# Kernel tuning notes

Hardware: AMD Instinct MI355X
Metric: run time of the kernel (lower is better)

## Reference

```python
import jax, jax.numpy as jnp
import numpy as np

S, B, V, E, H = 1024, 64, 32000, 512, 512
PAD = 0


def _ln3(x, g, b, eps=1e-5):
    # LayerNorm applied per-gate: x is (..., 3H); normalize over each H chunk.
    h = x.shape[-1] // 3
    xr = x.reshape(x.shape[:-1] + (3, h))
    mu = xr.mean(-1, keepdims=True)
    var = xr.var(-1, keepdims=True)
    xn = (xr - mu) * jax.lax.rsqrt(var + eps)
    out = xn * g.reshape(3, h) + b.reshape(3, h)
    return out.reshape(x.shape)


def _gru_dir(x, Wih, Whh, bih, bhh, gih, beih, ghh, behh, reverse):
    # x: (S, B, E). Precompute all input projections at once (big GEMM),
    # then scan the recurrence.
    xp = _ln3(jnp.einsum('sbe,ge->sbg', x, Wih), gih, beih) + bih  # (S,B,3H)

    def step(h, xt):
        hp = _ln3(h @ Whh.T, ghh, behh) + bhh  # (B,3H)
        xr, xz, xn = jnp.split(xt, 3, axis=-1)
        hr, hz, hn = jnp.split(hp, 3, axis=-1)
        r = jax.nn.sigmoid(xr + hr)
        z = jax.nn.sigmoid(xz + hz)
        n = jnp.tanh(xn + r * hn)
        hnew = (1.0 - z) * n + z * h
        return hnew, hnew

    h0 = jnp.zeros((x.shape[1], Whh.shape[1]), x.dtype)
    hT, ys = jax.lax.scan(step, h0, xp, reverse=reverse)
    return ys, hT  # ys in original time order for both directions


def setup_inputs() -> dict:
    key = jax.random.key(0)
    ks = jax.random.split(key, 8)
    sE = 1.0 / np.sqrt(E)
    sH = 1.0 / np.sqrt(H)
    z3 = jnp.zeros((3 * H,), jnp.float32)
    o3 = jnp.ones((3 * H,), jnp.float32)
    return {
        'src': jax.random.randint(ks[0], (S, B), 0, V, dtype=jnp.int32),
        'emb': jax.random.normal(ks[1], (V, E), jnp.float32),
        'W_ih_f': jax.random.normal(ks[2], (3 * H, E), jnp.float32) * sE,
        'W_hh_f': jax.random.normal(ks[3], (3 * H, H), jnp.float32) * sH,
        'b_ih_f': z3, 'b_hh_f': z3,
        'g_ih_f': o3, 'be_ih_f': z3, 'g_hh_f': o3, 'be_hh_f': z3,
        'W_ih_b': jax.random.normal(ks[4], (3 * H, E), jnp.float32) * sE,
        'W_hh_b': jax.random.normal(ks[5], (3 * H, H), jnp.float32) * sH,
        'b_ih_b': z3, 'b_hh_b': z3,
        'g_ih_b': o3, 'be_ih_b': z3, 'g_hh_b': o3, 'be_hh_b': z3,
        'W_out': jax.random.normal(ks[6], (H, 2 * H), jnp.float32) * (1.0 / np.sqrt(2 * H)),
        'b_out': jnp.zeros((H,), jnp.float32),
    }


def reference(src, emb, W_ih_f, W_hh_f, b_ih_f, b_hh_f, g_ih_f, be_ih_f,
              g_hh_f, be_hh_f, W_ih_b, W_hh_b, b_ih_b, b_hh_b, g_ih_b,
              be_ih_b, g_hh_b, be_hh_b, W_out, b_out):
    # Embedding with padding_idx=0 (padding row contributes zeros).
    x = emb[src] * (src != PAD)[..., None].astype(emb.dtype)  # (S,B,E)
    # embedding_dropout = dropout = 0.0 -> identity (eval semantics)
    yf, hf = _gru_dir(x, W_ih_f, W_hh_f, b_ih_f, b_hh_f,
                      g_ih_f, be_ih_f, g_hh_f, be_hh_f, reverse=False)
    yb, hb = _gru_dir(x, W_ih_b, W_hh_b, b_ih_b, b_hh_b,
                      g_ih_b, be_ih_b, g_hh_b, be_hh_b, reverse=True)
    gru_out = jnp.concatenate([yf, yb], axis=-1)  # (S,B,2H)
    outputs = jnp.tanh(gru_out @ W_out.T + b_out)  # (S,B,H)
    hidden = jnp.stack([hf, hb], axis=0)  # (2,B,H)
    return outputs, hidden
```

## Files before the change

### kernel.cpp

```cpp
#include <hip/hip_runtime.h>
#include <hip/hip_bf16.h>
#include <hip/hip_fp16.h>

#define S_ 1024
#define B_ 64
#define E_ 512
#define H_ 512
#define G3_ 1536

typedef __hip_bfloat16 bf16;
typedef __half f16;
typedef unsigned long long ULL;

template<typename T> struct alignas(4*sizeof(T)) V4 { T v[4]; };

__device__ __forceinline__ float toF(float x){ return x; }
__device__ __forceinline__ float toF(bf16 x){ return __bfloat162float(x); }
__device__ __forceinline__ float toF(f16 x){ return __half2float(x); }
__device__ __forceinline__ void storeF(float* p, float v){ *p = v; }
__device__ __forceinline__ void storeF(bf16* p, float v){ *p = __float2bfloat16(v); }
__device__ __forceinline__ void storeF(f16* p, float v){ *p = __float2half(v); }

__device__ __forceinline__ ULL cohLoad8(const ULL* p){
  return __hip_atomic_load(p, __ATOMIC_RELAXED, __HIP_MEMORY_SCOPE_AGENT);
}
__device__ __forceinline__ void cohStore4(float* p, float v){
  __hip_atomic_store(p, v, __ATOMIC_RELAXED, __HIP_MEMORY_SCOPE_AGENT);
}
__device__ __forceinline__ unsigned flagLoad(const unsigned* p){
  return __hip_atomic_load(p, __ATOMIC_RELAXED, __HIP_MEMORY_SCOPE_AGENT);
}
__device__ __forceinline__ void flagStore(unsigned* p, unsigned v){
  __hip_atomic_store(p, v, __ATOMIC_RELAXED, __HIP_MEMORY_SCOPE_AGENT);
}

__global__ __launch_bounds__(256)
void signal_kernel(float* __restrict__ out, long n, float v)
{
  long i = (long)blockIdx.x * 256 + threadIdx.x;
  const long stride = (long)gridDim.x * 256;
  for (; i < n; i += stride) out[i] = v;
}

template<typename XT, typename HT, int AMODE, int EPI>
__global__ __launch_bounds__(256, 2)
void gemm_tile(const int* __restrict__ src, const float* __restrict__ emb,
               const HT* __restrict__ Af, int rsF, const XT* __restrict__ Ab, int rsB,
               const float* __restrict__ W,
               XT* __restrict__ Cx, float* __restrict__ Cf, const float* __restrict__ bias,
               int N, int K)
{
  __shared__ float As[16][132];
  __shared__ float Bs[16][132];
  __shared__ int s_tok[128];
  const int m0 = blockIdx.x * 128;
  const int n0 = blockIdx.y * 128;
  const int tid = threadIdx.x;
  const int tx = tid & 15, ty = tid >> 4;

  if constexpr (AMODE == 0) {
    if (tid < 128) s_tok[tid] = src[m0 + tid];
  }
  __syncthreads();

  float acc[8][8];
  #pragma unroll
  for (int i = 0; i < 8; ++i)
    #pragma unroll
    for (int j = 0; j < 8; ++j) acc[i][j] = 0.f;

  for (int k0 = 0; k0 < K; k0 += 16) {
    #pragma unroll
    for (int i = 0; i < 2; ++i) {
      const int f = tid * 2 + i;
      const int r = f >> 2, kq = f & 3;
      const int kk = k0 + kq * 4;
      float a0, a1, a2, a3;
      if constexpr (AMODE == 0) {
        const int tok = s_tok[r];
        if (tok != 0) {
          float4 v = *(const float4*)(emb + (size_t)tok * E_ + kk);
          a0 = v.x; a1 = v.y; a2 = v.z; a3 = v.w;
        } else { a0 = a1 = a2 = a3 = 0.f; }
      } else {
        if (kk < H_) {
          V4<HT> v = *(const V4<HT>*)(Af + (size_t)(m0 + r) * rsF + kk);
          a0 = toF(v.v[0]); a1 = toF(v.v[1]); a2 = toF(v.v[2]); a3 = toF(v.v[3]);
        } else {
          V4<XT> v = *(const V4<XT>*)(Ab + (size_t)(m0 + r) * rsB + (kk - H_));
          a0 = toF(v.v[0]); a1 = toF(v.v[1]); a2 = toF(v.v[2]); a3 = toF(v.v[3]);
        }
      }
      As[kq*4+0][r] = a0; As[kq*4+1][r] = a1; As[kq*4+2][r] = a2; As[kq*4+3][r] = a3;
      float4 b = *(const float4*)(W + (size_t)(n0 + r) * K + kk);
      Bs[kq*4+0][r] = b.x; Bs[kq*4+1][r] = b.y; Bs[kq*4+2][r] = b.z; Bs[kq*4+3][r] = b.w;
    }
    __syncthreads();
    #pragma unroll
    for (int k = 0; k < 16; ++k) {
      float4 ra0 = *(const float4*)&As[k][ty*8];
      float4 ra1 = *(const float4*)&As[k][ty*8+4];
      float4 rb0 = *(const float4*)&Bs[k][tx*8];
      float4 rb1 = *(const float4*)&Bs[k][tx*8+4];
      float fa[8] = {ra0.x,ra0.y,ra0.z,ra0.w,ra1.x,ra1.y,ra1.z,ra1.w};
      float fb[8] = {rb0.x,rb0.y,rb0.z,rb0.w,rb1.x,rb1.y,rb1.z,rb1.w};
      #pragma unroll
      for (int i = 0; i < 8; ++i)
        #pragma unroll
        for (int j = 0; j < 8; ++j) acc[i][j] += fa[i] * fb[j];
    }
    __syncthreads();
  }

  if constexpr (EPI == 0) {
    #pragma unroll
    for (int i = 0; i < 8; ++i) {
      XT* crow = Cx + (size_t)(m0 + ty*8 + i) * N + n0 + tx*8;
      V4<XT> o0, o1;
      #pragma unroll
      for (int c = 0; c < 4; ++c) { storeF(&o0.v[c], acc[i][c]); storeF(&o1.v[c], acc[i][4+c]); }
      ((V4<XT>*)crow)[0] = o0; ((V4<XT>*)crow)[1] = o1;
    }
  } else {
    float bj[8];
    #pragma unroll
    for (int j = 0; j < 8; ++j) bj[j] = bias[n0 + tx*8 + j];
    #pragma unroll
    for (int i = 0; i < 8; ++i) {
      float* crow = Cf + (size_t)(m0 + ty*8 + i) * N + n0 + tx*8;
      float4 o0, o1;
      o0.x = tanhf(acc[i][0]+bj[0]); o0.y = tanhf(acc[i][1]+bj[1]);
      o0.z = tanhf(acc[i][2]+bj[2]); o0.w = tanhf(acc[i][3]+bj[3]);
      o1.x = tanhf(acc[i][4]+bj[4]); o1.y = tanhf(acc[i][5]+bj[5]);
      o1.z = tanhf(acc[i][6]+bj[6]); o1.w = tanhf(acc[i][7]+bj[7]);
      ((float4*)crow)[0] = o0; ((float4*)crow)[1] = o1;
    }
  }
}

template<typename XT>
__global__ __launch_bounds__(256)
void ln3_kernel(XT* __restrict__ xp, const float* __restrict__ g,
                const float* __restrict__ be, const float* __restrict__ b)
{
  const size_t base = (size_t)blockIdx.x * G3_;
  const int t = threadIdx.x;
  float v[6];
  #pragma unroll
  for (int gg = 0; gg < 3; ++gg) {
    v[gg*2+0] = toF(xp[base + gg*512 + t]);
    v[gg*2+1] = toF(xp[base + gg*512 + 256 + t]);
  }
  float s0 = v[0]+v[1], q0 = v[0]*v[0]+v[1]*v[1];
  float s1 = v[2]+v[3], q1 = v[2]*v[2]+v[3]*v[3];
  float s2 = v[4]+v[5], q2 = v[4]*v[4]+v[5]*v[5];
  #pragma unroll
  for (int m = 1; m < 64; m <<= 1) {
    s0 += __shfl_xor(s0, m); q0 += __shfl_xor(q0, m);
    s1 += __shfl_xor(s1, m); q1 += __shfl_xor(q1, m);
    s2 += __shfl_xor(s2, m); q2 += __shfl_xor(q2, m);
  }
  __shared__ float red[4][6];
  __shared__ float stat[6];
  const int wid = t >> 6, lane = t & 63;
  if (lane == 0) { red[wid][0]=s0; red[wid][1]=q0; red[wid][2]=s1; red[wid][3]=q1; red[wid][4]=s2; red[wid][5]=q2; }
  __syncthreads();
  if (t < 6) stat[t] = red[0][t] + red[1][t] + red[2][t] + red[3][t];
  __syncthreads();
  #pragma unroll
  for (int gg = 0; gg < 3; ++gg) {
    const float mu  = stat[gg*2]   * (1.f/512.f);
    const float var = stat[gg*2+1] * (1.f/512.f) - mu*mu;
    const float sc  = rsqrtf(var + 1e-5f);
    #pragma unroll
    for (int u = 0; u < 2; ++u) {
      const int c = gg*512 + u*256 + t;
      storeF(&xp[base + c], (v[gg*2+u] - mu) * sc * g[c] + be[c] + b[c]);
    }
  }
}

template<typename XT, typename HT>
__global__ __launch_bounds__(256, 2)
void scan_kernel(const XT* __restrict__ xp_f, const XT* __restrict__ xp_b,
                 const float* __restrict__ Whh_f, const float* __restrict__ Whh_b,
                 const float* __restrict__ gf, const float* __restrict__ bef, const float* __restrict__ bfv,
                 const float* __restrict__ gbv, const float* __restrict__ beb, const float* __restrict__ bbv,
                 float* __restrict__ hbuf, float* __restrict__ part,
                 unsigned* __restrict__ flags,
                 HT* __restrict__ houtF, int rsF, XT* __restrict__ houtB, int rsB,
                 float* __restrict__ outhid, int dirbase)
{
  __shared__ float hT[8][512];
  __shared__ float red[4][16][26];
  __shared__ float statL[48];
  __shared__ int sdead;

  const int bid  = blockIdx.x;
  const int gidx = dirbase*8 + (bid >> 5);
  const int dir  = gidx >> 3;
  const int bg   = gidx & 7;
  const int js   = bid & 31;
  const int tid  = threadIdx.x;
  const int jloc = tid & 15;
  const int pb   = tid >> 4;
  const int wid  = tid >> 6;
  const int ksw  = (tid >> 4) & 3;
  const int j    = js*16 + jloc;

  const XT* xp   = dir ? xp_b : xp_f;
  const float* W = dir ? Whh_b : Whh_f;
  const float* gv  = dir ? gbv : gf;
  const float* bev = dir ? beb : bef;
  const float* bv  = dir ? bbv : bfv;
  float* h = hbuf + dir * (B_ * H_);
  float* pgrp = part + (size_t)gidx * (48*32);
  unsigned* hfl = flags + (size_t)gidx * 2048;
  unsigned* sfl = hfl + 1024;

  if (tid == 0) sdead = 0;

  float w[3][32];
  {
    #pragma unroll
    for (int r = 0; r < 3; ++r) {
      const float* wr = W + (size_t)(r*H_ + j) * H_ + pb * 32;
      #pragma unroll
      for (int c = 0; c < 8; ++c) {
        const int p = (c + ksw*2) & 7;
        float4 f = *(const float4*)(wr + p*4);
        w[r][c*4+0] = f.x; w[r][c*4+1] = f.y; w[r][c*4+2] = f.z; w[r][c*4+3] = f.w;
      }
    }
  }
  const float gr0 = gv[j],            gr1 = gv[H_+j],               gr2 = gv[2*H_+j];
  const float gb0 = bev[j] + bv[j],   gb1 = bev[H_+j] + bv[H_+j],   gb2 = bev[2*H_+j] + bv[2*H_+j];
  __syncthreads();

  for (int t = 0; t < S_; ++t) {
    const int tf = dir ? (S_ - 1 - t) : t;
    float xr = 0.f, xz = 0.f, xn = 0.f;
    if (pb < 8) {
      const size_t xbase = ((size_t)tf * B_ + bg*8 + pb) * G3_;
      xr = toF(xp[xbase + j]);
      xz = toF(xp[xbase + H_ + j]);
      xn = toF(xp[xbase + 2*H_ + j]);
    }

    if (tid < 32 && !sdead) {
      const unsigned tgt = (unsigned)t;
      int guard = 0;
      while (flagLoad(&hfl[tid*32]) < tgt) {
        __builtin_amdgcn_s_sleep(1);
        if (++guard > (1 << 22)) { sdead = 1; break; }
      }
    }
    __syncthreads();

    {
      const int row = tid >> 5;
      const int seg = tid & 31;
      const ULL* hr = (const ULL*)(h + (size_t)(bg*8 + row) * H_);
      ULL v[8];
      #pragma unroll
      for (int i = 0; i < 8; ++i) v[i] = cohLoad8(hr + seg + i*32);
      ULL* dst = (ULL*)&hT[row][0];
      #pragma unroll
      for (int i = 0; i < 8; ++i) dst[seg + i*32] = v[i];
    }
    __syncthreads();

    for (int b = 0; b < 8; ++b) {
      float a0 = 0.f, a1 = 0.f, a2 = 0.f;
      #pragma unroll
      for (int c = 0; c < 8; ++c) {
        const int p = (c + ksw*2) & 7;
        const float4 hv = *(const float4*)&hT[b][pb*32 + p*4];
        a0 += hv.x*w[0][c*4+0] + hv.y*w[0][c*4+1] + hv.z*w[0][c*4+2] + hv.w*w[0][c*4+3];
        a1 += hv.x*w[1][c*4+0] + hv.y*w[1][c*4+1] + hv.z*w[1][c*4+2] + hv.w*w[1][c*4+3];
        a2 += hv.x*w[2][c*4+0] + hv.y*w[2][c*4+1] + hv.z*w[2][c*4+2] + hv.w*w[2][c*4+3];
      }
      a0 += __shfl_xor(a0, 16); a0 += __shfl_xor(a0, 32);
      a1 += __shfl_xor(a1, 16); a1 += __shfl_xor(a1, 32);
      a2 += __shfl_xor(a2, 16); a2 += __shfl_xor(a2, 32);
      if (ksw == 0) {
        red[wid][jloc][b*3+0] = a0; red[wid][jloc][b*3+1] = a1; red[wid][jloc][b*3+2] = a2;
      }
    }
    __syncthreads();

    float vr = 0.f, vz = 0.f, vn = 0.f;
    if (pb < 8) {
      vr = red[0][jloc][pb*3+0]+red[1][jloc][pb*3+0]+red[2][jloc][pb*3+0]+red[3][jloc][pb*3+0];
      vz = red[0][jloc][pb*3+1]+red[1][jloc][pb*3+1]+red[2][jloc][pb*3+1]+red[3][jloc][pb*3+1];
      vn = red[0][jloc][pb*3+2]+red[1][jloc][pb*3+2]+red[2][jloc][pb*3+2]+red[3][jloc][pb*3+2];

      float sr = vr, qr = vr*vr, sz = vz, qz = vz*vz, sn = vn, qn = vn*vn;
      #pragma unroll
      for (int m = 1; m < 16; m <<= 1) {
        sr += __shfl_xor(sr, m); qr += __shfl_xor(qr, m);
        sz += __shfl_xor(sz, m); qz += __shfl_xor(qz, m);
        sn += __shfl_xor(sn, m); qn += __shfl_xor(qn, m);
      }
      if (jloc == 0) {
        cohStore4(&pgrp[(pb*6+0)*32 + js], sr);
        cohStore4(&pgrp[(pb*6+1)*32 + js], qr);
        cohStore4(&pgrp[(pb*6+2)*32 + js], sz);
        cohStore4(&pgrp[(pb*6+3)*32 + js], qz);
        cohStore4(&pgrp[(pb*6+4)*32 + js], sn);
        cohStore4(&pgrp[(pb*6+5)*32 + js], qn);
      }
    }
    asm volatile("s_waitcnt vmcnt(0)" ::: "memory");
    __syncthreads();

    if (tid == 0) flagStore(&sfl[js*32], (unsigned)(t + 1));
    if (tid < 32 && !sdead) {
      const unsigned tgt = (unsigned)(t + 1);
      int guard = 0;
      while (flagLoad(&sfl[tid*32]) < tgt) {
        __builtin_amdgcn_s_sleep(1);
        if (++guard > (1 << 22)) { sdead = 1; break; }
      }
    }
    __syncthreads();

    if (tid < 48) {
      const ULL* prow = (const ULL*)(pgrp + tid * 32);
      float s = 0.f;
      #pragma unroll
      for (int u = 0; u < 16; ++u) {
        ULL v = cohLoad8(prow + u);
        union { ULL u64; float f[2]; } cv; cv.u64 = v;
        s += cv.f[0] + cv.f[1];
      }
      statL[tid] = s;
    }
    __syncthreads();

    if (pb < 8) {
      const int ab = bg*8 + pb;
      const float mur   = statL[pb*6+0]*(1.f/512.f);
      const float var_r = statL[pb*6+1]*(1.f/512.f) - mur*mur;
      const float muz   = statL[pb*6+2]*(1.f/512.f);
      const float var_z = statL[pb*6+3]*(1.f/512.f) - muz*muz;
      const float mun   = statL[pb*6+4]*(1.f/512.f);
      const float var_n = statL[pb*6+5]*(1.f/512.f) - mun*mun;
      const float hr_ = (vr - mur) * rsqrtf(var_r + 1e-5f) * gr0 + gb0;
      const float hz_ = (vz - muz) * rsqrtf(var_z + 1e-5f) * gr1 + gb1;
      const float hn_ = (vn - mun) * rsqrtf(var_n + 1e-5f) * gr2 + gb2;
      const float rg = 1.f / (1.f + __expf(-(xr + hr_)));
      const float zg = 1.f / (1.f + __expf(-(xz + hz_)));
      const float ng = tanhf(xn + rg * hn_);
      const float hprev = hT[pb][j];
      const float hnew = (1.f - zg) * ng + zg * hprev;
      cohStore4(&h[(size_t)ab * H_ + j], hnew);
      if (dir == 0) storeF(&houtF[((size_t)tf * B_ + ab) * rsF + j], hnew);
      else          storeF(&houtB[((size_t)tf * B_ + ab) * rsB + j], hnew);
      if (t == S_ - 1) outhid[((size_t)dir * B_ + ab) * H_ + j] = hnew;
    }
    asm volatile("s_waitcnt vmcnt(0)" ::: "memory");
    __syncthreads();
    if (tid == 0) flagStore(&hfl[js*32], (unsigned)(t + 1));
  }
}

static const size_t kCtrlBytes = 524288;
static const size_t kXpElems = (size_t)S_ * B_ * G3_;
static const size_t kHElems  = (size_t)S_ * B_ * H_;

struct Args {
  const int* src; const float* emb;
  const float *Wih_f, *Whh_f, *bih_f, *bhh_f, *gih_f, *beih_f, *ghh_f, *behh_f;
  const float *Wih_b, *Whh_b, *bih_b, *bhh_b, *gih_b, *beih_b, *ghh_b, *behh_b;
  const float *Wout, *bout;
  float* out; void* ws; hipStream_t stream;
};

template<typename XT>
static void run_parallel(const Args& a)
{
  float* hbuf = (float*)a.ws;
  float* part = hbuf + 65536;
  unsigned* flags = (unsigned*)(part + 24576);
  XT* xpf = (XT*)((char*)a.ws + kCtrlBytes);
  XT* xpb = xpf + kXpElems;
  float* outhid = a.out + kHElems;

  hipMemsetAsync(a.ws, 0, kCtrlBytes, a.stream);

  gemm_tile<XT,XT,0,0><<<dim3(512,12), dim3(256), 0, a.stream>>>(
      a.src, a.emb, (const XT*)nullptr, 0, (const XT*)nullptr, 0,
      a.Wih_f, xpf, nullptr, nullptr, G3_, E_);
  gemm_tile<XT,XT,0,0><<<dim3(512,12), dim3(256), 0, a.stream>>>(
      a.src, a.emb, (const XT*)nullptr, 0, (const XT*)nullptr, 0,
      a.Wih_b, xpb, nullptr, nullptr, G3_, E_);
  ln3_kernel<XT><<<dim3(S_*B_), dim3(256), 0, a.stream>>>(xpf, a.gih_f, a.beih_f, a.bih_f);
  ln3_kernel<XT><<<dim3(S_*B_), dim3(256), 0, a.stream>>>(xpb, a.gih_b, a.beih_b, a.bih_b);

  scan_kernel<XT,XT><<<dim3(512), dim3(256), 0, a.stream>>>(
      xpf, xpb, a.Whh_f, a.Whh_b, a.ghh_f, a.behh_f, a.bhh_f,
      a.ghh_b, a.behh_b, a.bhh_b, hbuf, part, flags,
      xpf, G3_, xpb, G3_, outhid, 0);

  gemm_tile<XT,XT,1,1><<<dim3(512,4), dim3(256), 0, a.stream>>>(
      nullptr, nullptr, xpf, G3_, xpb, G3_,
      a.Wout, (XT*)nullptr, a.out, a.bout, H_, 2*H_);
}

template<typename XT, typename HT>
static void run_sequential(const Args& a)
{
  float* hbuf = (float*)a.ws;
  float* part = hbuf + 65536;
  unsigned* flags = (unsigned*)(part + 24576);
  XT* xp = (XT*)((char*)a.ws + kCtrlBytes);
  HT* hf = (HT*)(xp + kXpElems);
  float* outhid = a.out + kHElems;

  hipMemsetAsync(a.ws, 0, kCtrlBytes, a.stream);

  gemm_tile<XT,XT,0,0><<<dim3(512,12), dim3(256), 0, a.stream>>>(
      a.src, a.emb, (const XT*)nullptr, 0, (const XT*)nullptr, 0,
      a.Wih_f, xp, nullptr, nullptr, G3_, E_);
  ln3_kernel<XT><<<dim3(S_*B_), dim3(256), 0, a.stream>>>(xp, a.gih_f, a.beih_f, a.bih_f);
  scan_kernel<XT,HT><<<dim3(256), dim3(256), 0, a.stream>>>(
      xp, xp, a.Whh_f, a.Whh_b, a.ghh_f, a.behh_f, a.bhh_f,
      a.ghh_b, a.behh_b, a.bhh_b, hbuf, part, flags,
      hf, H_, xp, G3_, outhid, 0);

  gemm_tile<XT,XT,0,0><<<dim3(512,12), dim3(256), 0, a.stream>>>(
      a.src, a.emb, (const XT*)nullptr, 0, (const XT*)nullptr, 0,
      a.Wih_b, xp, nullptr, nullptr, G3_, E_);
  ln3_kernel<XT><<<dim3(S_*B_), dim3(256), 0, a.stream>>>(xp, a.gih_b, a.beih_b, a.bih_b);
  scan_kernel<XT,HT><<<dim3(256), dim3(256), 0, a.stream>>>(
      xp, xp, a.Whh_f, a.Whh_b, a.ghh_f, a.behh_f, a.bhh_f,
      a.ghh_b, a.behh_b, a.bhh_b, hbuf, part, flags,
      hf, H_, xp, G3_, outhid, 1);

  gemm_tile<XT,HT,1,1><<<dim3(512,4), dim3(256), 0, a.stream>>>(
      nullptr, nullptr, hf, H_, xp, G3_,
      a.Wout, (XT*)nullptr, a.out, a.bout, H_, 2*H_);
}

extern "C" void kernel_launch(void* const* d_in, const int* in_sizes, int n_in,
                              void* d_out, int out_size, void* d_ws, size_t ws_size,
                              hipStream_t stream)
{
  Args a;
  a.src    = (const int*)  d_in[0];
  a.emb    = (const float*)d_in[1];
  a.Wih_f  = (const float*)d_in[2];
  a.Whh_f  = (const float*)d_in[3];
  a.bih_f  = (const float*)d_in[4];
  a.bhh_f  = (const float*)d_in[5];
  a.gih_f  = (const float*)d_in[6];
  a.beih_f = (const float*)d_in[7];
  a.ghh_f  = (const float*)d_in[8];
  a.behh_f = (const float*)d_in[9];
  a.Wih_b  = (const float*)d_in[10];
  a.Whh_b  = (const float*)d_in[11];
  a.bih_b  = (const float*)d_in[12];
  a.bhh_b  = (const float*)d_in[13];
  a.gih_b  = (const float*)d_in[14];
  a.beih_b = (const float*)d_in[15];
  a.ghh_b  = (const float*)d_in[16];
  a.behh_b = (const float*)d_in[17];
  a.Wout   = (const float*)d_in[18];
  a.bout   = (const float*)d_in[19];
  a.out = (float*)d_out;
  a.ws = d_ws;
  a.stream = stream;

  int dev = 0, cus = 0;
  hipGetDevice(&dev);
  hipDeviceGetAttribute(&cus, hipDeviceAttributeMultiprocessorCount, dev);

  const size_t needP = kCtrlBytes + 2*kXpElems*2;
  const size_t needS = kCtrlBytes + kXpElems*2 + kHElems*2;

  const bool sane = (n_in == 20) && (in_sizes[0] == S_*B_) && (in_sizes[1] == 32000*E_)
                 && (in_sizes[3] == G3_*H_) && (in_sizes[18] == H_*2*H_);

  float sigv = 0.f;
  bool ran = false;
  if (!sane) {
    sigv = 20000.f + (float)n_in;
  } else if (cus < 256) {
    sigv = 100000.f + (float)cus;
  } else if (ws_size >= needP) { run_parallel<f16>(a);        ran = true; }
  else if (ws_size >= needS) { run_sequential<f16,f16>(a);    ran = true; }
  else {
    unsigned wsMB = (unsigned)(ws_size >> 20);
    if (wsMB > 998) wsMB = 998;
    sigv = 1000.f + (float)wsMB;
  }

  if (!ran) {
    signal_kernel<<<dim3(1024), dim3(256), 0, stream>>>(a.out, (long)out_size, sigv);
  } else {
    hipError_t e = hipGetLastError();
    if (e != hipSuccess) {
      signal_kernel<<<dim3(1024), dim3(256), 0, stream>>>(a.out, (long)out_size,
                                                          10000.f + (float)(int)e);
    }
  }
}
```

Before: 13.34 ms.

## Replace FP32 SIMT GEMMs with FP16 MFMA GEMMs over pre-converted weights

Adds a conversion kernel that casts the embedding table, input-projection weights and output weights to fp16 in workspace on every call. The GEMM is rewritten to feed half8 fragments straight from global memory into 16x16x32 f16 MFMA instructions, with no shared-memory staging. This targets the FP32 FMA cost of the input-projection and output GEMMs. In exchange it adds per-call conversion traffic (the embedding table is large), needs a bigger workspace, loses precision by using fp16 operands, and its uncoalesced scalar epilogue stores may be slow.

```diff
diff --git a/kernel.cpp b/kernel.cpp
--- a/kernel.cpp
+++ b/kernel.cpp
@@ -7,10 +7,14 @@
 #define E_ 512
 #define H_ 512
 #define G3_ 1536
+#define V_ 32000
 
 typedef __hip_bfloat16 bf16;
 typedef __half f16;
 typedef unsigned long long ULL;
+
+typedef _Float16 half8 __attribute__((ext_vector_type(8)));
+typedef float f32x4v __attribute__((ext_vector_type(4)));
 
 template<typename T> struct alignas(4*sizeof(T)) V4 { T v[4]; };
 
@@ -42,98 +46,120 @@
   for (; i < n; i += stride) out[i] = v;
 }
 
-template<typename XT, typename HT, int AMODE, int EPI>
-__global__ __launch_bounds__(256, 2)
-void gemm_tile(const int* __restrict__ src, const float* __restrict__ emb,
-               const HT* __restrict__ Af, int rsF, const XT* __restrict__ Ab, int rsB,
-               const float* __restrict__ W,
-               XT* __restrict__ Cx, float* __restrict__ Cf, const float* __restrict__ bias,
-               int N, int K)
-{
-  __shared__ float As[16][132];
-  __shared__ float Bs[16][132];
+__global__ __launch_bounds__(256)
+void convF2H(const float* __restrict__ in, f16* __restrict__ out, long n)
+{
+  long i = ((long)blockIdx.x * 256 + threadIdx.x) * 8;
+  const long stride = (long)gridDim.x * 256 * 8;
+  for (; i < n; i += stride) {
+    float4 a = *(const float4*)(in + i);
+    float4 b = *(const float4*)(in + i + 4);
+    half8 o;
+    o[0] = (_Float16)a.x; o[1] = (_Float16)a.y; o[2] = (_Float16)a.z; o[3] = (_Float16)a.w;
+    o[4] = (_Float16)b.x; o[5] = (_Float16)b.y; o[6] = (_Float16)b.z; o[7] = (_Float16)b.w;
+    *(half8*)((_Float16*)out + i) = o;
+  }
+}
+
+template<int GMODE, int EPI>
+__global__ __launch_bounds__(256)
+void gemm16(const int* __restrict__ src, const f16* __restrict__ embh,
+            const f16* __restrict__ Af, int rsF,
+            const f16* __restrict__ Ab, int rsB,
+            const f16* __restrict__ Wh,
+            f16* __restrict__ Cx, float* __restrict__ Cf,
+            const float* __restrict__ bias, int N, int K)
+{
   __shared__ int s_tok[128];
+  const int tid = threadIdx.x;
   const int m0 = blockIdx.x * 128;
   const int n0 = blockIdx.y * 128;
-  const int tid = threadIdx.x;
-  const int tx = tid & 15, ty = tid >> 4;
-
-  if constexpr (AMODE == 0) {
+  const int wid = tid >> 6, lane = tid & 63;
+  const int wr = wid >> 1, wc = wid & 1;
+  const int lr = lane & 15, lg = lane >> 4;
+
+  if constexpr (GMODE == 0) {
     if (tid < 128) s_tok[tid] = src[m0 + tid];
   }
   __syncthreads();
 
-  float acc[8][8];
+  f32x4v acc[4][4];
   #pragma unroll
-  for (int i = 0; i < 8; ++i)
-    #pragma unroll
-    for (int j = 0; j < 8; ++j) acc[i][j] = 0.f;
-
-  for (int k0 = 0; k0 < K; k0 += 16) {
-    #pragma unroll
-    for (int i = 0; i < 2; ++i) {
-      const int f = tid * 2 + i;
-      const int r = f >> 2, kq = f & 3;
-      const int kk = k0 + kq * 4;
-      float a0, a1, a2, a3;
-      if constexpr (AMODE == 0) {
-        const int tok = s_tok[r];
-        if (tok != 0) {
-          float4 v = *(const float4*)(emb + (size_t)tok * E_ + kk);
-          a0 = v.x; a1 = v.y; a2 = v.z; a3 = v.w;
-        } else { a0 = a1 = a2 = a3 = 0.f; }
+  for (int i = 0; i < 4; ++i)
+    #pragma unroll
+    for (int j = 0; j < 4; ++j) {
+      acc[i][j][0] = 0.f; acc[i][j][1] = 0.f; acc[i][j][2] = 0.f; acc[i][j][3] = 0.f;
+    }
+
+  int atok[4]; size_t abase[4];
+  #pragma unroll
+  for (int i = 0; i < 4; ++i) {
+    const int lm = wr*64 + i*16 + lr;
+    if constexpr (GMODE == 0) {
+      const int tok = s_tok[lm];
+      atok[i] = tok;
+      abase[i] = (size_t)tok * K;
+    } else {
+      atok[i] = m0 + lm;
+      abase[i] = 0;
+    }
+  }
+  const half8 zero8 = {};
+
+  for (int k0 = 0; k0 < K; k0 += 32) {
+    const int kk = k0 + lg*8;
+    half8 afr[4], bfr[4];
+    #pragma unroll
+    for (int i = 0; i < 4; ++i) {
+      if constexpr (GMODE == 0) {
+        afr[i] = *(const half8*)((const _Float16*)embh + abase[i] + kk);
+        if (atok[i] == 0) afr[i] = zero8;
       } else {
-        if (kk < H_) {
-          V4<HT> v = *(const V4<HT>*)(Af + (size_t)(m0 + r) * rsF + kk);
-          a0 = toF(v.v[0]); a1 = toF(v.v[1]); a2 = toF(v.v[2]); a3 = toF(v.v[3]);
-        } else {
-          V4<XT> v = *(const V4<XT>*)(Ab + (size_t)(m0 + r) * rsB + (kk - H_));
-          a0 = toF(v.v[0]); a1 = toF(v.v[1]); a2 = toF(v.v[2]); a3 = toF(v.v[3]);
+        const int m = atok[i];
+        const _Float16* p = (kk < 512)
+            ? ((const _Float16*)Af + (size_t)m * rsF + kk)
+            : ((const _Float16*)Ab + (size_t)m * rsB + (kk - 512));
+        afr[i] = *(const half8*)p;
+      }
+    }
+    #pragma unroll
+    for (int j = 0; j < 4; ++j) {
+      const int n = n0 + wc*64 + j*16 + lr;
+      bfr[j] = *(const half8*)((const _Float16*)Wh + (size_t)n * K + kk);
+    }
+    #pragma unroll
+    for (int i = 0; i < 4; ++i)
+      #pragma unroll
+      for (int j = 0; j < 4; ++j)
+        acc[i][j] = __builtin_amdgcn_mfma_f32_16x16x32_f16(afr[i], bfr[j], acc[i][j], 0, 0, 0);
+  }
+
+  if constexpr (EPI == 0) {
+    #pragma unroll
+    for (int i = 0; i < 4; ++i) {
+      #pragma unroll
+      for (int j = 0; j < 4; ++j) {
+        const int n = n0 + wc*64 + j*16 + lr;
+        #pragma unroll
+        for (int r = 0; r < 4; ++r) {
+          const int m = m0 + wr*64 + i*16 + lg*4 + r;
+          Cx[(size_t)m * N + n] = __float2half(acc[i][j][r]);
         }
       }
-      As[kq*4+0][r] = a0; As[kq*4+1][r] = a1; As[kq*4+2][r] = a2; As[kq*4+3][r] = a3;
-      float4 b = *(const float4*)(W + (size_t)(n0 + r) * K + kk);
-      Bs[kq*4+0][r] = b.x; Bs[kq*4+1][r] = b.y; Bs[kq*4+2][r] = b.z; Bs[kq*4+3][r] = b.w;
-    }
-    __syncthreads();
-    #pragma unroll
-    for (int k = 0; k < 16; ++k) {
-      float4 ra0 = *(const float4*)&As[k][ty*8];
-      float4 ra1 = *(const float4*)&As[k][ty*8+4];
-      float4 rb0 = *(const float4*)&Bs[k][tx*8];
-      float4 rb1 = *(const float4*)&Bs[k][tx*8+4];
-      float fa[8] = {ra0.x,ra0.y,ra0.z,ra0.w,ra1.x,ra1.y,ra1.z,ra1.w};
-      float fb[8] = {rb0.x,rb0.y,rb0.z,rb0.w,rb1.x,rb1.y,rb1.z,rb1.w};
-      #pragma unroll
-      for (int i = 0; i < 8; ++i)
+    }
+  } else {
+    #pragma unroll
+    for (int j = 0; j < 4; ++j) {
+      const int n = n0 + wc*64 + j*16 + lr;
+      const float bj = bias[n];
+      #pragma unroll
+      for (int i = 0; i < 4; ++i) {
         #pragma unroll
-        for (int j = 0; j < 8; ++j) acc[i][j] += fa[i] * fb[j];
-    }
-    __syncthreads();
-  }
-
-  if constexpr (EPI == 0) {
-    #pragma unroll
-    for (int i = 0; i < 8; ++i) {
-      XT* crow = Cx + (size_t)(m0 + ty*8 + i) * N + n0 + tx*8;
-      V4<XT> o0, o1;
-      #pragma unroll
-      for (int c = 0; c < 4; ++c) { storeF(&o0.v[c], acc[i][c]); storeF(&o1.v[c], acc[i][4+c]); }
-      ((V4<XT>*)crow)[0] = o0; ((V4<XT>*)crow)[1] = o1;
-    }
-  } else {
-    float bj[8];
-    #pragma unroll
-    for (int j = 0; j < 8; ++j) bj[j] = bias[n0 + tx*8 + j];
-    #pragma unroll
-    for (int i = 0; i < 8; ++i) {
-      float* crow = Cf + (size_t)(m0 + ty*8 + i) * N + n0 + tx*8;
-      float4 o0, o1;
-      o0.x = tanhf(acc[i][0]+bj[0]); o0.y = tanhf(acc[i][1]+bj[1]);
-      o0.z = tanhf(acc[i][2]+bj[2]); o0.w = tanhf(acc[i][3]+bj[3]);
-      o1.x = tanhf(acc[i][4]+bj[4]); o1.y = tanhf(acc[i][5]+bj[5]);
-      o1.z = tanhf(acc[i][6]+bj[6]); o1.w = tanhf(acc[i][7]+bj[7]);
-      ((float4*)crow)[0] = o0; ((float4*)crow)[1] = o1;
+        for (int r = 0; r < 4; ++r) {
+          const int m = m0 + wr*64 + i*16 + lg*4 + r;
+          Cf[(size_t)m * N + n] = tanhf(acc[i][j][r] + bj);
+        }
+      }
     }
   }
 }
@@ -368,6 +394,9 @@
 static const size_t kCtrlBytes = 524288;
 static const size_t kXpElems = (size_t)S_ * B_ * G3_;
 static const size_t kHElems  = (size_t)S_ * B_ * H_;
+static const size_t kEmbElems  = (size_t)V_ * E_;
+static const size_t kWihElems  = (size_t)G3_ * E_;
+static const size_t kWoutElems = (size_t)H_ * 2 * H_;
 
 struct Args {
   const int* src; const float* emb;
@@ -377,70 +406,86 @@
   float* out; void* ws; hipStream_t stream;
 };
 
-template<typename XT>
 static void run_parallel(const Args& a)
 {
   float* hbuf = (float*)a.ws;
   float* part = hbuf + 65536;
   unsigned* flags = (unsigned*)(part + 24576);
-  XT* xpf = (XT*)((char*)a.ws + kCtrlBytes);
-  XT* xpb = xpf + kXpElems;
+  f16* xpf = (f16*)((char*)a.ws + kCtrlBytes);
+  f16* xpb = xpf + kXpElems;
+  f16* emb16 = xpb + kXpElems;
+  f16* w16f = emb16 + kEmbElems;
+  f16* w16b = w16f + kWihElems;
+  f16* wout16 = w16b + kWihElems;
   float* outhid = a.out + kHElems;
 
   hipMemsetAsync(a.ws, 0, kCtrlBytes, a.stream);
 
-  gemm_tile<XT,XT,0,0><<<dim3(512,12), dim3(256), 0, a.stream>>>(
-      a.src, a.emb, (const XT*)nullptr, 0, (const XT*)nullptr, 0,
-      a.Wih_f, xpf, nullptr, nullptr, G3_, E_);
-  gemm_tile<XT,XT,0,0><<<dim3(512,12), dim3(256), 0, a.stream>>>(
-      a.src, a.emb, (const XT*)nullptr, 0, (const XT*)nullptr, 0,
-      a.Wih_b, xpb, nullptr, nullptr, G3_, E_);
-  ln3_kernel<XT><<<dim3(S_*B_), dim3(256), 0, a.stream>>>(xpf, a.gih_f, a.beih_f, a.bih_f);
-  ln3_kernel<XT><<<dim3(S_*B_), dim3(256), 0, a.stream>>>(xpb, a.gih_b, a.beih_b, a.bih_b);
-
-  scan_kernel<XT,XT><<<dim3(512), dim3(256), 0, a.stream>>>(
+  convF2H<<<dim3(1024), dim3(256), 0, a.stream>>>(a.emb, emb16, (long)kEmbElems);
+  convF2H<<<dim3(256), dim3(256), 0, a.stream>>>(a.Wih_f, w16f, (long)kWihElems);
+  convF2H<<<dim3(256), dim3(256), 0, a.stream>>>(a.Wih_b, w16b, (long)kWihElems);
+  convF2H<<<dim3(256), dim3(256), 0, a.stream>>>(a.Wout, wout16, (long)kWoutElems);
+
+  gemm16<0,0><<<dim3(512,12), dim3(256), 0, a.stream>>>(
+      a.src, emb16, (const f16*)nullptr, 0, (const f16*)nullptr, 0,
+      w16f, xpf, nullptr, nullptr, G3_, E_);
+  gemm16<0,0><<<dim3(512,12), dim3(256), 0, a.stream>>>(
+      a.src, emb16, (const f16*)nullptr, 0, (const f16*)nullptr, 0,
+      w16b, xpb, nullptr, nullptr, G3_, E_);
+  ln3_kernel<f16><<<dim3(S_*B_), dim3(256), 0, a.stream>>>(xpf, a.gih_f, a.beih_f, a.bih_f);
+  ln3_kernel<f16><<<dim3(S_*B_), dim3(256), 0, a.stream>>>(xpb, a.gih_b, a.beih_b, a.bih_b);
+
+  scan_kernel<f16,f16><<<dim3(512), dim3(256), 0, a.stream>>>(
       xpf, xpb, a.Whh_f, a.Whh_b, a.ghh_f, a.behh_f, a.bhh_f,
       a.ghh_b, a.behh_b, a.bhh_b, hbuf, part, flags,
       xpf, G3_, xpb, G3_, outhid, 0);
 
-  gemm_tile<XT,XT,1,1><<<dim3(512,4), dim3(256), 0, a.stream>>>(
+  gemm16<1,1><<<dim3(512,4), dim3(256), 0, a.stream>>>(
       nullptr, nullptr, xpf, G3_, xpb, G3_,
-      a.Wout, (XT*)nullptr, a.out, a.bout, H_, 2*H_);
-}
-
-template<typename XT, typename HT>
+      wout16, nullptr, a.out, a.bout, H_, 2*H_);
+}
+
 static void run_sequential(const Args& a)
 {
   float* hbuf = (float*)a.ws;
   float* part = hbuf + 65536;
   unsigned* flags = (unsigned*)(part + 24576);
-  XT* xp = (XT*)((char*)a.ws + kCtrlBytes);
-  HT* hf = (HT*)(xp + kXpElems);
+  f16* xp = (f16*)((char*)a.ws + kCtrlBytes);
+  f16* hf = xp + kXpElems;
+  f16* emb16 = hf + kHElems;
+  f16* w16f = emb16 + kEmbElems;
+  f16* w16b = w16f + kWihElems;
+  f16* wout16 = w16b + kWihElems;
   float* outhid = a.out + kHElems;
 
   hipMemsetAsync(a.ws, 0, kCtrlBytes, a.stream);
 
-  gemm_tile<XT,XT,0,0><<<dim3(512,12), dim3(256), 0, a.stream>>>(
-      a.src, a.emb, (const XT*)nullptr, 0, (const XT*)nullptr, 0,
-      a.Wih_f, xp, nullptr, nullptr, G3_, E_);
-  ln3_kernel<XT><<<dim3(S_*B_), dim3(256), 0, a.stream>>>(xp, a.gih_f, a.beih_f, a.bih_f);
-  scan_kernel<XT,HT><<<dim3(256), dim3(256), 0, a.stream>>>(
+  convF2H<<<dim3(1024), dim3(256), 0, a.stream>>>(a.emb, emb16, (long)kEmbElems);
+  convF2H<<<dim3(256), dim3(256), 0, a.stream>>>(a.Wih_f, w16f, (long)kWihElems);
+  convF2H<<<dim3(256), dim3(256), 0, a.stream>>>(a.Wih_b, w16b, (long)kWihElems);
+  convF2H<<<dim3(256), dim3(256), 0, a.stream>>>(a.Wout, wout16, (long)kWoutElems);
+
+  gemm16<0,0><<<dim3(512,12), dim3(256), 0, a.stream>>>(
+      a.src, emb16, (const f16*)nullptr, 0, (const f16*)nullptr, 0,
+      w16f, xp, nullptr, nullptr, G3_, E_);
+  ln3_kernel<f16><<<dim3(S_*B_), dim3(256), 0, a.stream>>>(xp, a.gih_f, a.beih_f, a.bih_f);
+  scan_kernel<f16,f16><<<dim3(256), dim3(256), 0, a.stream>>>(
       xp, xp, a.Whh_f, a.Whh_b, a.ghh_f, a.behh_f, a.bhh_f,
       a.ghh_b, a.behh_b, a.bhh_b, hbuf, part, flags,
       hf, H_, xp, G3_, outhid, 0);
 
-  gemm_tile<XT,XT,0,0><<<dim3(512,12), dim3(256), 0, a.stream>>>(
-      a.src, a.emb, (const XT*)nullptr, 0, (const XT*)nullptr, 0,
-      a.Wih_b, xp, nullptr, nullptr, G3_, E_);
-  ln3_kernel<XT><<<dim3(S_*B_), dim3(256), 0, a.stream>>>(xp, a.gih_b, a.beih_b, a.bih_b);
-  scan_kernel<XT,HT><<<dim3(256), dim3(256), 0, a.stream>>>(
+  gemm16<0,0><<<dim3(512,12), dim3(256), 0, a.stream>>>(
+      a.src, emb16, (const f16*)nullptr, 0, (const f16*)nullptr, 0,
+      w16b, xp, nullptr, nullptr, G3_, E_);
+  ln3_kernel<f16><<<dim3(S_*B_), dim3(256), 0, a.stream>>>(xp, a.gih_b, a.beih_b, a.bih_b);
+  scan_kernel<f16,f16><<<dim3(256), dim3(256), 0, a.stream>>>(
       xp, xp, a.Whh_f, a.Whh_b, a.ghh_f, a.behh_f, a.bhh_f,
       a.ghh_b, a.behh_b, a.bhh_b, hbuf, part, flags,
       hf, H_, xp, G3_, outhid, 1);
 
-  gemm_tile<XT,HT,1,1><<<dim3(512,4), dim3(256), 0, a.stream>>>(
+  gemm16<1,1><<<dim3(512,4), dim3(256), 0, a.stream>>>(
       nullptr, nullptr, hf, H_, xp, G3_,
-      a.Wout, (XT*)nullptr, a.out, a.bout, H_, 2*H_);
+      wout16, nullptr, a.out, a.bout, H_, 2*H_);
 }
 
 extern "C" void kernel_launch(void* const* d_in, const int* in_sizes, int n_in,
@@ -476,10 +521,11 @@
   hipGetDevice(&dev);
   hipDeviceGetAttribute(&cus, hipDeviceAttributeMultiprocessorCount, dev);
 
-  const size_t needP = kCtrlBytes + 2*kXpElems*2;
-  const size_t needS = kCtrlBytes + kXpElems*2 + kHElems*2;
-
-  const bool sane = (n_in == 20) && (in_sizes[0] == S_*B_) && (in_sizes[1] == 32000*E_)
+  const size_t extraElems = kEmbElems + 2*kWihElems + kWoutElems;
+  const size_t needP = kCtrlBytes + (2*kXpElems + extraElems) * 2;
+  const size_t needS = kCtrlBytes + (kXpElems + kHElems + extraElems) * 2;
+
+  const bool sane = (n_in == 20) && (in_sizes[0] == S_*B_) && (in_sizes[1] == V_*E_)
                  && (in_sizes[3] == G3_*H_) && (in_sizes[18] == H_*2*H_);
 
   float sigv = 0.f;
@@ -488,8 +534,8 @@
     sigv = 20000.f + (float)n_in;
   } else if (cus < 256) {
     sigv = 100000.f + (float)cus;
-  } else if (ws_size >= needP) { run_parallel<f16>(a);        ran = true; }
-  else if (ws_size >= needS) { run_sequential<f16,f16>(a);    ran = true; }
+  } else if (ws_size >= needP) { run_parallel(a);   ran = true; }
+  else if (ws_size >= needS)   { run_sequential(a); ran = true; }
   else {
     unsigned wsMB = (unsigned)(ws_size >> 20);
     if (wsMB > 998) wsMB = 998;
```

Measured after the change: 10.83 ms (median of 4 runs). -18.8%, faster.
